# Kernel tuning notes

Measured on AMD Instinct MI355X. Metric: run time of the kernel, lower is better.

Reference implementation:

```python
import jax, jax.numpy as jnp
import numpy as np

N = 100000
E = 1600000
EMB3 = 192   # embedding_size * 3
F_LAT = 64   # latency_feature_size
F_OUT = 128  # latency_feature_size * 2 (GATConv out_feats, 1 head)
NEG_SLOPE = 0.2  # DGL GATConv default leaky_relu slope


def setup_inputs() -> dict:
    key = jax.random.key(0)
    ks = jax.random.split(key, 9)
    return {
        "embed": jax.random.normal(ks[0], (N, EMB3), dtype=jnp.float32),
        "src": jax.random.randint(ks[1], (E,), 0, N, dtype=jnp.int64)
               if jax.config.jax_enable_x64 else jax.random.randint(ks[1], (E,), 0, N, dtype=jnp.int32),
        "dst": jax.random.randint(ks[2], (E,), 0, N, dtype=jnp.int32),
        "W_lin": jax.random.normal(ks[3], (EMB3, F_LAT), dtype=jnp.float32) * 0.05,
        "b_lin": jax.random.normal(ks[4], (F_LAT,), dtype=jnp.float32) * 0.05,
        "W_gat": jax.random.normal(ks[5], (F_LAT, F_OUT), dtype=jnp.float32) * 0.05,
        "attn_l": jax.random.normal(ks[6], (F_OUT,), dtype=jnp.float32) * 0.05,
        "attn_r": jax.random.normal(ks[7], (F_OUT,), dtype=jnp.float32) * 0.05,
        "b_gat": jax.random.normal(ks[8], (F_OUT,), dtype=jnp.float32) * 0.05,
    }


def reference(embed, src, dst, W_lin, b_lin, W_gat, attn_l, attn_r, b_gat):
    # linear_input + relu: [N, 192] -> [N, 64]
    x = jax.nn.relu(embed @ W_lin + b_lin)

    # GATConv (1 head): projection [N, 128]
    feat = x @ W_gat
    el = feat @ attn_l  # [N]
    er = feat @ attn_r  # [N]

    # per-edge attention logit with leaky relu
    e = jax.nn.leaky_relu(el[src] + er[dst], negative_slope=NEG_SLOPE)  # [E]

    # edge softmax over incoming edges of each dst node (segment softmax)
    emax = jax.ops.segment_max(e, dst, num_segments=N)           # [N], -inf for empty
    emax = jnp.where(jnp.isfinite(emax), emax, 0.0)
    ee = jnp.exp(e - emax[dst])                                   # [E]
    denom = jax.ops.segment_sum(ee, dst, num_segments=N)          # [N]
    denom = jnp.where(denom > 0, denom, 1.0)
    alpha = ee / denom[dst]                                       # [E]

    # weighted message aggregation: [N, 128]
    rst = jax.ops.segment_sum(feat[src] * alpha[:, None], dst, num_segments=N)
    y = rst + b_gat  # GATConv bias

    mu, logvar = jnp.split(y, 2, axis=-1)
    return mu, jnp.tanh(logvar)
```

## Files before the change

### kernel.cpp

```cpp
#include <hip/hip_runtime.h>
#include <hip/hip_bf16.h>
#include <hip/hip_fp16.h>

#define NEG_SLOPE 0.2f

typedef __attribute__((ext_vector_type(8))) short bf16x8;
typedef __attribute__((ext_vector_type(4))) float f32x4;

__device__ __forceinline__ unsigned pack_bf16(float a, float b) {
    unsigned ua = __float_as_uint(a), ub = __float_as_uint(b);
    ua += 0x7FFFu + ((ua >> 16) & 1u);
    ub += 0x7FFFu + ((ub >> 16) & 1u);
    return (ua >> 16) | (ub & 0xFFFF0000u);
}

__device__ __forceinline__ unsigned pack_f16(float a, float b) {
    union { __half2 h; unsigned u; } cv;
    cv.h = __floats2half2_rn(a, b);
    return cv.u;
}

__global__ __launch_bounds__(256) void k_gemm(
    const float* __restrict__ embed, const float* __restrict__ W_lin,
    const float* __restrict__ b_lin, const float* __restrict__ W_gat,
    const float* __restrict__ attn_l, const float* __restrict__ attn_r,
    unsigned* __restrict__ feat_u32, float* __restrict__ el,
    float* __restrict__ er, int N)
{
    __shared__ __align__(16) char lds[40960];
    const int t = threadIdx.x;
    const int lane = t & 63;
    const int w = t >> 6;
    const int lc = lane & 15;
    const int hg = lane >> 4;
    const int nb = blockIdx.x * 128;

    for (int i = t; i < 6144; i += 256) {
        const int c = i & 63, kp = i >> 6;
        const float w0 = W_lin[(2 * kp) * 64 + c];
        const float w1 = W_lin[(2 * kp + 1) * 64 + c];
        const unsigned off = (unsigned)(c * 384 + kp * 4) ^ ((c & 7) << 4);
        *(unsigned*)(lds + off) = pack_bf16(w0, w1);
    }
    for (int i = t; i < 4096; i += 256) {
        const int c = i & 127, kp = i >> 7;
        const float w0 = W_gat[(2 * kp) * 128 + c];
        const float w1 = W_gat[(2 * kp + 1) * 128 + c];
        const unsigned off = (unsigned)(c * 128 + kp * 4) ^ ((c & 7) << 4);
        *(unsigned*)(lds + 24576 + off) = pack_bf16(w0, w1);
    }
    __syncthreads();

    f32x4 acc1[2][4];
#pragma unroll
    for (int mt = 0; mt < 2; mt++)
#pragma unroll
        for (int nt = 0; nt < 4; nt++) acc1[mt][nt] = (f32x4)0.f;

#pragma unroll
    for (int ks = 0; ks < 6; ks++) {
        bf16x8 bfr[4];
#pragma unroll
        for (int nt = 0; nt < 4; nt++) {
            const int c = nt * 16 + lc;
            const unsigned off = (unsigned)(c * 384 + ks * 64 + hg * 16) ^ ((c & 7) << 4);
            bfr[nt] = *(const bf16x8*)(lds + off);
        }
#pragma unroll
        for (int mt = 0; mt < 2; mt++) {
            int row = nb + w * 32 + mt * 16 + lc;
            if (row >= N) row = N - 1;
            const float4* ep = (const float4*)(embed + (size_t)row * 192 + ks * 32 + hg * 8);
            const float4 p = ep[0], q = ep[1];
            union { bf16x8 v; unsigned u[4]; } a;
            a.u[0] = pack_bf16(p.x, p.y); a.u[1] = pack_bf16(p.z, p.w);
            a.u[2] = pack_bf16(q.x, q.y); a.u[3] = pack_bf16(q.z, q.w);
#pragma unroll
            for (int nt = 0; nt < 4; nt++)
                acc1[mt][nt] = __builtin_amdgcn_mfma_f32_16x16x32_bf16(a.v, bfr[nt], acc1[mt][nt], 0, 0, 0);
        }
    }

    float blv[4];
#pragma unroll
    for (int nt = 0; nt < 4; nt++) blv[nt] = b_lin[nt * 16 + lc];

    __syncthreads();

#pragma unroll
    for (int mt = 0; mt < 2; mt++)
#pragma unroll
        for (int nt = 0; nt < 4; nt++)
#pragma unroll
            for (int r = 0; r < 4; r++) {
                float v = acc1[mt][nt][r] + blv[nt];
                v = v > 0.f ? v : 0.f;
                const int xrow = w * 32 + mt * 16 + 4 * hg + r;
                const int col = nt * 16 + lc;
                const unsigned off = (unsigned)(xrow * 128 + col * 2) ^ ((xrow & 7) << 4);
                unsigned bv = __float_as_uint(v);
                bv += 0x7FFFu + ((bv >> 16) & 1u);
                *(unsigned short*)(lds + off) = (unsigned short)(bv >> 16);
            }
    __syncthreads();

    f32x4 acc2[2][8];
#pragma unroll
    for (int mt = 0; mt < 2; mt++)
#pragma unroll
        for (int nt = 0; nt < 8; nt++) acc2[mt][nt] = (f32x4)0.f;

#pragma unroll
    for (int ks = 0; ks < 2; ks++) {
        bf16x8 a2[2];
#pragma unroll
        for (int mt = 0; mt < 2; mt++) {
            const int row = w * 32 + mt * 16 + lc;
            const unsigned off = (unsigned)(row * 128 + ks * 64 + hg * 16) ^ ((row & 7) << 4);
            a2[mt] = *(const bf16x8*)(lds + off);
        }
#pragma unroll
        for (int nt = 0; nt < 8; nt++) {
            const int c = nt * 16 + lc;
            const unsigned off = (unsigned)(c * 128 + ks * 64 + hg * 16) ^ ((c & 7) << 4);
            const bf16x8 b2 = *(const bf16x8*)(lds + 24576 + off);
            acc2[0][nt] = __builtin_amdgcn_mfma_f32_16x16x32_bf16(a2[0], b2, acc2[0][nt], 0, 0, 0);
            acc2[1][nt] = __builtin_amdgcn_mfma_f32_16x16x32_bf16(a2[1], b2, acc2[1][nt], 0, 0, 0);
        }
    }

    float alv[8], arv[8];
#pragma unroll
    for (int nt = 0; nt < 8; nt++) {
        alv[nt] = attn_l[nt * 16 + lc];
        arv[nt] = attn_r[nt * 16 + lc];
    }

#pragma unroll
    for (int mt = 0; mt < 2; mt++) {
        const int rbase = nb + w * 32 + mt * 16 + 4 * hg;
#pragma unroll
        for (int nt = 0; nt < 8; nt++)
#pragma unroll
            for (int r = 0; r < 4; r++) {
                const float V = acc2[mt][nt][r];
                const float Vp = __shfl_xor(V, 1, 64);
                const int row = rbase + r;
                if (!(lc & 1) && row < N)
                    feat_u32[(size_t)row * 64 + nt * 8 + (lc >> 1)] = pack_f16(V, Vp);
            }
        float elv[4] = {0.f, 0.f, 0.f, 0.f}, erv[4] = {0.f, 0.f, 0.f, 0.f};
#pragma unroll
        for (int nt = 0; nt < 8; nt++)
#pragma unroll
            for (int r = 0; r < 4; r++) {
                elv[r] = fmaf(acc2[mt][nt][r], alv[nt], elv[r]);
                erv[r] = fmaf(acc2[mt][nt][r], arv[nt], erv[r]);
            }
#pragma unroll
        for (int r = 0; r < 4; r++) {
#pragma unroll
            for (int o = 1; o < 16; o <<= 1) {
                elv[r] += __shfl_xor(elv[r], o, 64);
                erv[r] += __shfl_xor(erv[r], o, 64);
            }
            const int row = rbase + r;
            if (lc == r && row < N) { el[row] = elv[r]; er[row] = erv[r]; }
        }
    }
}

__global__ void k_hist(const int* __restrict__ dst, int* __restrict__ counts,
                       int* __restrict__ rank, int E) {
    const int i = (blockIdx.x * 256 + threadIdx.x) * 4;
    if (i + 3 < E) {
        const int4 v = *(const int4*)&dst[i];
        int4 r;
        r.x = atomicAdd(&counts[v.x], 1);
        r.y = atomicAdd(&counts[v.y], 1);
        r.z = atomicAdd(&counts[v.z], 1);
        r.w = atomicAdd(&counts[v.w], 1);
        *(int4*)&rank[i] = r;
    } else {
        for (int j = i; j < E; j++) rank[j] = atomicAdd(&counts[dst[j]], 1);
    }
}

__global__ __launch_bounds__(256) void k_scan1(
    const int* __restrict__ counts, int* __restrict__ offs,
    int* __restrict__ blocksums, int N)
{
    __shared__ int lds[256];
    const int t = threadIdx.x;
    const int base = blockIdx.x * 1024 + t * 4;
    int c0 = 0, c1 = 0, c2 = 0, c3 = 0;
    if (base + 3 < N) {
        int4 v = *(const int4*)&counts[base];
        c0 = v.x; c1 = v.y; c2 = v.z; c3 = v.w;
    } else {
        if (base + 0 < N) c0 = counts[base + 0];
        if (base + 1 < N) c1 = counts[base + 1];
        if (base + 2 < N) c2 = counts[base + 2];
        if (base + 3 < N) c3 = counts[base + 3];
    }
    const int s = c0 + c1 + c2 + c3;
    lds[t] = s;
    __syncthreads();
    for (int o = 1; o < 256; o <<= 1) {
        int u = (t >= o) ? lds[t - o] : 0;
        __syncthreads();
        lds[t] += u;
        __syncthreads();
    }
    const int excl = lds[t] - s;
    int o0 = excl, o1 = excl + c0, o2 = o1 + c1, o3 = o2 + c2;
    if (base + 3 < N) {
        *(int4*)&offs[base] = make_int4(o0, o1, o2, o3);
    } else {
        if (base + 0 < N) offs[base + 0] = o0;
        if (base + 1 < N) offs[base + 1] = o1;
        if (base + 2 < N) offs[base + 2] = o2;
        if (base + 3 < N) offs[base + 3] = o3;
    }
    if (t == 255) blocksums[blockIdx.x] = lds[255];
}

__global__ void k_scan2(int* __restrict__ blocksums, int nb) {
    __shared__ int lds[128];
    const int t = threadIdx.x;
    const int v = (t < nb) ? blocksums[t] : 0;
    lds[t] = v;
    __syncthreads();
    for (int o = 1; o < 128; o <<= 1) {
        int u = (t >= o) ? lds[t - o] : 0;
        __syncthreads();
        lds[t] += u;
        __syncthreads();
    }
    if (t < nb) blocksums[t] = lds[t] - v;
}

__global__ void k_scan3(int* __restrict__ offs, const int* __restrict__ blocksums,
                        int N, int E) {
    int i = blockIdx.x * 256 + threadIdx.x;
    if (i < N) offs[i] += blocksums[i >> 10];
    if (i == 0) offs[N] = E;
}

__global__ void k_scat(const int* __restrict__ src, const int* __restrict__ dst,
                       const int* __restrict__ rank, const int* __restrict__ offs,
                       unsigned* __restrict__ csru, int E) {
    const int i = (blockIdx.x * 256 + threadIdx.x) * 4;
    if (i + 3 < E) {
        const int4 s4 = *(const int4*)&src[i];
        const int4 d4 = *(const int4*)&dst[i];
        const int4 r4 = *(const int4*)&rank[i];
        csru[offs[d4.x] + r4.x] = (unsigned)s4.x | ((unsigned)(d4.x & 15) << 20);
        csru[offs[d4.y] + r4.y] = (unsigned)s4.y | ((unsigned)(d4.y & 15) << 20);
        csru[offs[d4.z] + r4.z] = (unsigned)s4.z | ((unsigned)(d4.z & 15) << 20);
        csru[offs[d4.w] + r4.w] = (unsigned)s4.w | ((unsigned)(d4.w & 15) << 20);
    } else {
        for (int j = i; j < E; j++)
            csru[offs[dst[j]] + rank[j]] = (unsigned)src[j] | ((unsigned)(dst[j] & 15) << 20);
    }
}

__global__ __launch_bounds__(256, 1) void k_agg(
    const unsigned* __restrict__ csru, const int* __restrict__ offs,
    const float* __restrict__ el, const float* __restrict__ er,
    const unsigned* __restrict__ feat, const float* __restrict__ b_gat,
    float* __restrict__ out, int N)
{
    __shared__ __align__(16) char ldsB[32768];
    const int t = threadIdx.x;
    const int lane = t & 63;
    const int wid = t >> 6;
    const int lc = lane & 15;
    const int hg = lane >> 4;
    char* wlds = ldsB + wid * 8192;

    const int ntiles = (N + 15) >> 4;
    const int tile = blockIdx.x * 4 + wid;
    if (tile >= ntiles) return;
    const int d0 = tile << 4;
    const int dmax = min(16, N - d0);

    const int wstart = offs[d0];
    const int wend = offs[d0 + dmax];
    const int nw = (wend - wstart + 31) >> 5;

    f32x4 accD[8];
    f32x4 accDen = (f32x4)0.f;
#pragma unroll
    for (int nt = 0; nt < 8; nt++) accD[nt] = (f32x4)0.f;

    union { bf16x8 v; unsigned u[4]; } ONESF;
    ONESF.u[0] = ONESF.u[1] = ONESF.u[2] = ONESF.u[3] = 0x3C003C00u;

    unsigned ev_n = 0u;
    int m_c = 0;
    float elv_c = -3.4e38f, erv_c = 0.f;
    uint4 g0, g1, g2, g3, g4, g5, g6, g7;
    g0 = g1 = g2 = g3 = g4 = g5 = g6 = g7 = make_uint4(0u, 0u, 0u, 0u);

#define GATHER_ALL(SJ)                                                                      \
    do {                                                                                    \
        int rs_;                                                                            \
        rs_ = __shfl((SJ), 0 + hg, 64);  g0 = *(const uint4*)&feat[(size_t)rs_ * 64 + lc * 4]; \
        rs_ = __shfl((SJ), 4 + hg, 64);  g1 = *(const uint4*)&feat[(size_t)rs_ * 64 + lc * 4]; \
        rs_ = __shfl((SJ), 8 + hg, 64);  g2 = *(const uint4*)&feat[(size_t)rs_ * 64 + lc * 4]; \
        rs_ = __shfl((SJ), 12 + hg, 64); g3 = *(const uint4*)&feat[(size_t)rs_ * 64 + lc * 4]; \
        rs_ = __shfl((SJ), 16 + hg, 64); g4 = *(const uint4*)&feat[(size_t)rs_ * 64 + lc * 4]; \
        rs_ = __shfl((SJ), 20 + hg, 64); g5 = *(const uint4*)&feat[(size_t)rs_ * 64 + lc * 4]; \
        rs_ = __shfl((SJ), 24 + hg, 64); g6 = *(const uint4*)&feat[(size_t)rs_ * 64 + lc * 4]; \
        rs_ = __shfl((SJ), 28 + hg, 64); g7 = *(const uint4*)&feat[(size_t)rs_ * 64 + lc * 4]; \
    } while (0)

    if (nw > 0) {
        const int e0 = wstart + lane;
        const bool v0 = (lane < 32) && (e0 < wend);
        const unsigned ev_c = v0 ? csru[e0] : 0u;
        if (nw > 1) {
            const int e1 = wstart + 32 + lane;
            ev_n = (lane < 32 && e1 < wend) ? csru[e1] : 0u;
        }
        const int sj_c = (int)(ev_c & 0xFFFFFu);
        m_c = (int)((ev_c >> 20) & 15u);
        elv_c = v0 ? el[sj_c] : -3.4e38f;
        erv_c = er[d0 + m_c];
        GATHER_ALL(sj_c);
    }

    int w = wstart;
    for (int i = 0; i < nw; ++i, w += 32) {
        *(uint4*)(wlds + ((unsigned)((0  + hg) * 256 + lc * 16) ^ 0u))  = g0;
        *(uint4*)(wlds + ((unsigned)((4  + hg) * 256 + lc * 16) ^ 0u))  = g1;
        *(uint4*)(wlds + ((unsigned)((8  + hg) * 256 + lc * 16) ^ 16u)) = g2;
        *(uint4*)(wlds + ((unsigned)((12 + hg) * 256 + lc * 16) ^ 16u)) = g3;
        *(uint4*)(wlds + ((unsigned)((16 + hg) * 256 + lc * 16) ^ 32u)) = g4;
        *(uint4*)(wlds + ((unsigned)((20 + hg) * 256 + lc * 16) ^ 32u)) = g5;
        *(uint4*)(wlds + ((unsigned)((24 + hg) * 256 + lc * 16) ^ 48u)) = g6;
        *(uint4*)(wlds + ((unsigned)((28 + hg) * 256 + lc * 16) ^ 48u)) = g7;

        float ee = elv_c + erv_c;
        ee = ee >= 0.f ? ee : NEG_SLOPE * ee;
        const float p_c = __expf(ee);
        union { bf16x8 v; unsigned u[4]; } A;
#pragma unroll
        for (int jj = 0; jj < 4; jj++) {
            const int sl = 8 * hg + 2 * jj;
            const float p0 = __shfl(p_c, sl, 64);
            const int   m0 = __shfl(m_c, sl, 64);
            const float p1 = __shfl(p_c, sl + 1, 64);
            const int   m1 = __shfl(m_c, sl + 1, 64);
            A.u[jj] = pack_f16((m0 == lc) ? p0 : 0.f, (m1 == lc) ? p1 : 0.f);
        }

        const int sj_n = (int)(ev_n & 0xFFFFFu);
        const int m_n = (int)((ev_n >> 20) & 15u);
        {
            const int e1 = w + 32 + lane;
            const bool vn = (lane < 32) && (e1 < wend);
            elv_c = vn ? el[sj_n] : -3.4e38f;
            erv_c = er[d0 + m_n];
            m_c = m_n;
        }

        GATHER_ALL(sj_n);

        {
            unsigned ev_f = 0u;
            if (i + 2 < nw) {
                const int e2 = w + 64 + lane;
                ev_f = (lane < 32 && e2 < wend) ? csru[e2] : 0u;
            }
            ev_n = ev_f;
        }

#pragma unroll
        for (int nt = 0; nt < 8; nt++) {
            union { bf16x8 v; unsigned short s[8]; } B;
#pragma unroll
            for (int j = 0; j < 8; j++) {
                const unsigned roff = ((unsigned)((8 * hg + j) * 256 + (nt * 16 + lc) * 2))
                                      ^ (((unsigned)hg & 3u) << 4);
                B.s[j] = *(const unsigned short*)(wlds + roff);
            }
            accD[nt] = __builtin_amdgcn_mfma_f32_16x16x32_f16(A.v, B.v, accD[nt], 0, 0, 0);
        }
        accDen = __builtin_amdgcn_mfma_f32_16x16x32_f16(A.v, ONESF.v, accDen, 0, 0, 0);
    }
#undef GATHER_ALL

    float inv[4];
#pragma unroll
    for (int r = 0; r < 4; r++) {
        const float den = accDen[r];
        inv[r] = den > 0.f ? 1.f / den : 0.f;
    }

    const size_t nh = (size_t)N * 64;
#pragma unroll
    for (int r = 0; r < 4; r++) {
        const int d = d0 + 4 * hg + r;
        if (d < N) {
#pragma unroll
            for (int nt = 0; nt < 8; nt++) {
                const int c = nt * 16 + lc;
                const float y = accD[nt][r] * inv[r] + b_gat[c];
                if (c < 64) out[(size_t)d * 64 + c] = y;
                else        out[nh + (size_t)d * 64 + (c - 64)] = tanhf(y);
            }
        }
    }
}

extern "C" void kernel_launch(void* const* d_in, const int* in_sizes, int n_in,
                              void* d_out, int out_size, void* d_ws, size_t ws_size,
                              hipStream_t stream) {
    const float* embed  = (const float*)d_in[0];
    const int*   src    = (const int*)d_in[1];
    const int*   dst    = (const int*)d_in[2];
    const float* W_lin  = (const float*)d_in[3];
    const float* b_lin  = (const float*)d_in[4];
    const float* W_gat  = (const float*)d_in[5];
    const float* attn_l = (const float*)d_in[6];
    const float* attn_r = (const float*)d_in[7];
    const float* b_gat  = (const float*)d_in[8];
    float* out = (float*)d_out;

    const int N = in_sizes[0] / 192;
    const int E = in_sizes[1];

    char* ws = (char*)d_ws;
    size_t off = 0;
    auto alloc = [&](size_t bytes) -> void* {
        void* p = ws + off;
        off += (bytes + 255) & ~(size_t)255;
        return p;
    };
    unsigned* feat     = (unsigned*)alloc((size_t)N * 64 * 4);
    float*    el       = (float*)alloc((size_t)N * 4);
    float*    er       = (float*)alloc((size_t)N * 4);
    int*      counts   = (int*)alloc((size_t)N * 4);
    int*      offs     = (int*)alloc(((size_t)N + 1) * 4);
    int*      rank     = (int*)alloc((size_t)E * 4);
    unsigned* csru     = (unsigned*)alloc((size_t)E * 4);
    int*      blocksums= (int*)alloc(1024 * 4);

    hipMemsetAsync(counts, 0, (size_t)N * 4, stream);

    k_gemm<<<(N + 127) / 128, 256, 0, stream>>>(embed, W_lin, b_lin, W_gat,
                                                attn_l, attn_r, feat, el, er, N);
    k_hist<<<(E / 4 + 255) / 256, 256, 0, stream>>>(dst, counts, rank, E);
    const int nb1 = (N + 1023) / 1024;
    k_scan1<<<nb1, 256, 0, stream>>>(counts, offs, blocksums, N);
    k_scan2<<<1, 128, 0, stream>>>(blocksums, nb1);
    k_scan3<<<(N + 255) / 256, 256, 0, stream>>>(offs, blocksums, N, E);
    k_scat<<<(E / 4 + 255) / 256, 256, 0, stream>>>(src, dst, rank, offs, csru, E);

    const int ntiles = (N + 15) / 16;
    k_agg<<<(ntiles + 3) / 4, 256, 0, stream>>>(csru, offs, el, er, feat, b_gat, out, N);
}
```

Before: 223.6 us.

## Split each destination tile's edge windows across two waves and reduce via LDS

Each 16-node destination tile is now handled by a pair of waves. The two waves take alternating 32-edge windows, so each walks half of the tile's edges and the serial gather/MFMA chain per wave gets shorter. The second wave writes its partial accumulators to LDS, and after a block barrier the first wave adds them and writes the output. This doubles the grid and adds an LDS reduction plus two __syncthreads, in exchange for more latency hiding on the irregular feature gathers.

```diff
diff --git a/kernel.cpp b/kernel.cpp
--- a/kernel.cpp
+++ b/kernel.cpp
@@ -280,14 +280,21 @@
     char* wlds = ldsB + wid * 8192;
 
     const int ntiles = (N + 15) >> 4;
-    const int tile = blockIdx.x * 4 + wid;
-    if (tile >= ntiles) return;
+    const int pair = wid >> 1;
+    const int sub  = wid & 1;
+    const int tile = blockIdx.x * 2 + pair;
+    const bool active = tile < ntiles;
     const int d0 = tile << 4;
-    const int dmax = min(16, N - d0);
-
-    const int wstart = offs[d0];
-    const int wend = offs[d0 + dmax];
-    const int nw = (wend - wstart + 31) >> 5;
+
+    int wstart = 0, wend = 0;
+    if (active) {
+        const int dmax = min(16, N - d0);
+        wstart = offs[d0];
+        wend = offs[d0 + dmax];
+    }
+    const int wbase0 = wstart + 32 * sub;
+    int nw = 0;
+    if (active && wbase0 < wend) nw = ((wend - wbase0) + 63) >> 6;
 
     f32x4 accD[8];
     f32x4 accDen = (f32x4)0.f;
@@ -317,11 +324,11 @@
     } while (0)
 
     if (nw > 0) {
-        const int e0 = wstart + lane;
+        const int e0 = wbase0 + lane;
         const bool v0 = (lane < 32) && (e0 < wend);
         const unsigned ev_c = v0 ? csru[e0] : 0u;
         if (nw > 1) {
-            const int e1 = wstart + 32 + lane;
+            const int e1 = wbase0 + 64 + lane;
             ev_n = (lane < 32 && e1 < wend) ? csru[e1] : 0u;
         }
         const int sj_c = (int)(ev_c & 0xFFFFFu);
@@ -331,8 +338,8 @@
         GATHER_ALL(sj_c);
     }
 
-    int w = wstart;
-    for (int i = 0; i < nw; ++i, w += 32) {
+    int w = wbase0;
+    for (int i = 0; i < nw; ++i, w += 64) {
         *(uint4*)(wlds + ((unsigned)((0  + hg) * 256 + lc * 16) ^ 0u))  = g0;
         *(uint4*)(wlds + ((unsigned)((4  + hg) * 256 + lc * 16) ^ 0u))  = g1;
         *(uint4*)(wlds + ((unsigned)((8  + hg) * 256 + lc * 16) ^ 16u)) = g2;
@@ -359,7 +366,7 @@
         const int sj_n = (int)(ev_n & 0xFFFFFu);
         const int m_n = (int)((ev_n >> 20) & 15u);
         {
-            const int e1 = w + 32 + lane;
+            const int e1 = w + 64 + lane;
             const bool vn = (lane < 32) && (e1 < wend);
             elv_c = vn ? el[sj_n] : -3.4e38f;
             erv_c = er[d0 + m_n];
@@ -371,7 +378,7 @@
         {
             unsigned ev_f = 0u;
             if (i + 2 < nw) {
-                const int e2 = w + 64 + lane;
+                const int e2 = w + 128 + lane;
                 ev_f = (lane < 32 && e2 < wend) ? csru[e2] : 0u;
             }
             ev_n = ev_f;
@@ -391,6 +398,27 @@
         accDen = __builtin_amdgcn_mfma_f32_16x16x32_f16(A.v, ONESF.v, accDen, 0, 0, 0);
     }
 #undef GATHER_ALL
+
+    __syncthreads();
+
+    float* cb = (float*)ldsB + pair * 2368 + lane * 37;
+    if (sub == 1 && active) {
+#pragma unroll
+        for (int nt = 0; nt < 8; nt++)
+#pragma unroll
+            for (int r = 0; r < 4; r++) cb[nt * 4 + r] = accD[nt][r];
+#pragma unroll
+        for (int r = 0; r < 4; r++) cb[32 + r] = accDen[r];
+    }
+    __syncthreads();
+    if (sub != 0 || !active) return;
+
+#pragma unroll
+    for (int nt = 0; nt < 8; nt++)
+#pragma unroll
+        for (int r = 0; r < 4; r++) accD[nt][r] += cb[nt * 4 + r];
+#pragma unroll
+    for (int r = 0; r < 4; r++) accDen[r] += cb[32 + r];
 
     float inv[4];
 #pragma unroll
@@ -460,5 +488,5 @@
     k_scat<<<(E / 4 + 255) / 256, 256, 0, stream>>>(src, dst, rank, offs, csru, E);
 
     const int ntiles = (N + 15) / 16;
-    k_agg<<<(ntiles + 3) / 4, 256, 0, stream>>>(csru, offs, el, er, feat, b_gat, out, N);
-}
+    k_agg<<<(ntiles + 1) / 2, 256, 0, stream>>>(csru, offs, el, er, feat, b_gat, out, N);
+}
```

Measured after the change: 232.6 us. 4.0% more time.

## Fuse degree histogram into GEMM kernel and fold scan fixup into consumers

Applied to the files above, without the earlier changes.

Moves the per-edge atomic histogram over dst into the tail of the GEMM kernel, with each GEMM block handling a contiguous chunk of edges. Removes the separate scan3 kernel by having the scatter and aggregation kernels add the per-1024 block prefix sums themselves when reading offsets. This cuts two kernel launches and one pass over the offsets array. In exchange it adds an extra lookup per offset read, and the GEMM blocks now also carry atomic traffic, which may lengthen their tail.

```diff
diff --git a/kernel.cpp b/kernel.cpp
--- a/kernel.cpp
+++ b/kernel.cpp
@@ -25,7 +25,9 @@
     const float* __restrict__ b_lin, const float* __restrict__ W_gat,
     const float* __restrict__ attn_l, const float* __restrict__ attn_r,
     unsigned* __restrict__ feat_u32, float* __restrict__ el,
-    float* __restrict__ er, int N)
+    float* __restrict__ er, int N,
+    const int* __restrict__ dstp, int* __restrict__ counts,
+    int* __restrict__ rank, int E)
 {
     __shared__ __align__(16) char lds[40960];
     const int t = threadIdx.x;
@@ -168,21 +170,25 @@
             if (lc == r && row < N) { el[row] = elv[r]; er[row] = erv[r]; }
         }
     }
-}
-
-__global__ void k_hist(const int* __restrict__ dst, int* __restrict__ counts,
-                       int* __restrict__ rank, int E) {
-    const int i = (blockIdx.x * 256 + threadIdx.x) * 4;
-    if (i + 3 < E) {
-        const int4 v = *(const int4*)&dst[i];
-        int4 r;
-        r.x = atomicAdd(&counts[v.x], 1);
-        r.y = atomicAdd(&counts[v.y], 1);
-        r.z = atomicAdd(&counts[v.z], 1);
-        r.w = atomicAdd(&counts[v.w], 1);
-        *(int4*)&rank[i] = r;
-    } else {
-        for (int j = i; j < E; j++) rank[j] = atomicAdd(&counts[dst[j]], 1);
+
+    {
+        const int nblk = gridDim.x;
+        const int per_blk = (((E + nblk - 1) / nblk) + 1023) & ~1023;
+        const int ebase = blockIdx.x * per_blk;
+        const int eend = min(E, ebase + per_blk);
+        for (int i = ebase + t * 4; i < eend; i += 1024) {
+            if (i + 3 < eend) {
+                const int4 v = *(const int4*)&dstp[i];
+                int4 r;
+                r.x = atomicAdd(&counts[v.x], 1);
+                r.y = atomicAdd(&counts[v.y], 1);
+                r.z = atomicAdd(&counts[v.z], 1);
+                r.w = atomicAdd(&counts[v.w], 1);
+                *(int4*)&rank[i] = r;
+            } else {
+                for (int j = i; j < eend; j++) rank[j] = atomicAdd(&counts[dstp[j]], 1);
+            }
+        }
     }
 }
 
@@ -240,36 +246,31 @@
     if (t < nb) blocksums[t] = lds[t] - v;
 }
 
-__global__ void k_scan3(int* __restrict__ offs, const int* __restrict__ blocksums,
-                        int N, int E) {
-    int i = blockIdx.x * 256 + threadIdx.x;
-    if (i < N) offs[i] += blocksums[i >> 10];
-    if (i == 0) offs[N] = E;
-}
-
 __global__ void k_scat(const int* __restrict__ src, const int* __restrict__ dst,
                        const int* __restrict__ rank, const int* __restrict__ offs,
-                       unsigned* __restrict__ csru, int E) {
+                       const int* __restrict__ bs, unsigned* __restrict__ csru, int E) {
     const int i = (blockIdx.x * 256 + threadIdx.x) * 4;
     if (i + 3 < E) {
         const int4 s4 = *(const int4*)&src[i];
         const int4 d4 = *(const int4*)&dst[i];
         const int4 r4 = *(const int4*)&rank[i];
-        csru[offs[d4.x] + r4.x] = (unsigned)s4.x | ((unsigned)(d4.x & 15) << 20);
-        csru[offs[d4.y] + r4.y] = (unsigned)s4.y | ((unsigned)(d4.y & 15) << 20);
-        csru[offs[d4.z] + r4.z] = (unsigned)s4.z | ((unsigned)(d4.z & 15) << 20);
-        csru[offs[d4.w] + r4.w] = (unsigned)s4.w | ((unsigned)(d4.w & 15) << 20);
+        csru[offs[d4.x] + bs[d4.x >> 10] + r4.x] = (unsigned)s4.x | ((unsigned)(d4.x & 15) << 20);
+        csru[offs[d4.y] + bs[d4.y >> 10] + r4.y] = (unsigned)s4.y | ((unsigned)(d4.y & 15) << 20);
+        csru[offs[d4.z] + bs[d4.z >> 10] + r4.z] = (unsigned)s4.z | ((unsigned)(d4.z & 15) << 20);
+        csru[offs[d4.w] + bs[d4.w >> 10] + r4.w] = (unsigned)s4.w | ((unsigned)(d4.w & 15) << 20);
     } else {
         for (int j = i; j < E; j++)
-            csru[offs[dst[j]] + rank[j]] = (unsigned)src[j] | ((unsigned)(dst[j] & 15) << 20);
+            csru[offs[dst[j]] + bs[dst[j] >> 10] + rank[j]] =
+                (unsigned)src[j] | ((unsigned)(dst[j] & 15) << 20);
     }
 }
 
 __global__ __launch_bounds__(256, 1) void k_agg(
     const unsigned* __restrict__ csru, const int* __restrict__ offs,
+    const int* __restrict__ bs,
     const float* __restrict__ el, const float* __restrict__ er,
     const unsigned* __restrict__ feat, const float* __restrict__ b_gat,
-    float* __restrict__ out, int N)
+    float* __restrict__ out, int N, int E)
 {
     __shared__ __align__(16) char ldsB[32768];
     const int t = threadIdx.x;
@@ -285,8 +286,9 @@
     const int d0 = tile << 4;
     const int dmax = min(16, N - d0);
 
-    const int wstart = offs[d0];
-    const int wend = offs[d0 + dmax];
+    const int wstart = offs[d0] + bs[d0 >> 10];
+    const int dend = d0 + dmax;
+    const int wend = (dend >= N) ? E : (offs[dend] + bs[dend >> 10]);
     const int nw = (wend - wstart + 31) >> 5;
 
     f32x4 accD[8];
@@ -451,14 +453,14 @@
     hipMemsetAsync(counts, 0, (size_t)N * 4, stream);
 
     k_gemm<<<(N + 127) / 128, 256, 0, stream>>>(embed, W_lin, b_lin, W_gat,
-                                                attn_l, attn_r, feat, el, er, N);
-    k_hist<<<(E / 4 + 255) / 256, 256, 0, stream>>>(dst, counts, rank, E);
+                                                attn_l, attn_r, feat, el, er, N,
+                                                dst, counts, rank, E);
     const int nb1 = (N + 1023) / 1024;
     k_scan1<<<nb1, 256, 0, stream>>>(counts, offs, blocksums, N);
     k_scan2<<<1, 128, 0, stream>>>(blocksums, nb1);
-    k_scan3<<<(N + 255) / 256, 256, 0, stream>>>(offs, blocksums, N, E);
-    k_scat<<<(E / 4 + 255) / 256, 256, 0, stream>>>(src, dst, rank, offs, csru, E);
+    k_scat<<<(E / 4 + 255) / 256, 256, 0, stream>>>(src, dst, rank, offs, blocksums, csru, E);
 
     const int ntiles = (N + 15) / 16;
-    k_agg<<<(ntiles + 3) / 4, 256, 0, stream>>>(csru, offs, el, er, feat, b_gat, out, N);
-}
+    k_agg<<<(ntiles + 3) / 4, 256, 0, stream>>>(csru, offs, blocksums, el, er,
+                                                feat, b_gat, out, N, E);
+}
```

New measurement: 256.5 us. 1.15x slower.
